# Kernel tuning notes

Hardware: AMD Instinct MI355X
Metric: run time of the kernel (lower is better)

Reference implementation:

```python
import jax, jax.numpy as jnp
import numpy as np

B, P, D, N = 16, 128, 256, 256  # batch, patches, channels (d), features (n); d <= n required


def setup_inputs() -> dict:
    key = jax.random.key(0)
    k1, k2, k3, k4 = jax.random.split(key, 4)
    x = jax.random.normal(k1, (B, P, D, N), dtype=jnp.float32)
    # Linear(n, 1) weights stacked over the d layers: W[i] is the i-th layer's weight row.
    bound = 1.0 / np.sqrt(N)
    W = jax.random.uniform(k2, (D, N), dtype=jnp.float32, minval=-bound, maxval=bound)
    bias = jax.random.uniform(k3, (D,), dtype=jnp.float32, minval=-bound, maxval=bound)
    # Each row of perm is an independent random permutation of [0, N) (matches torch.randperm per row).
    perm = jnp.argsort(jax.random.uniform(k4, (D, N)), axis=1).astype(jnp.int32)
    return {"x": x, "W": W, "bias": bias, "perm": perm}


def reference(x, W, bias, perm):
    # x: [b,p,d,n]; gather along last axis with a per-channel permutation: xp[b,p,i,k] = x[b,p,i,perm[i,k]]
    xp = jnp.take_along_axis(x, perm[None, None, :, :].astype(jnp.int32), axis=3)
    # Linear_i(n -> 1): y[b,p,i] = sum_k xp[b,p,i,k] * W[i,k] + bias[i]
    y = jnp.einsum('bpdn,dn->bpd', xp, W) + bias
    # The original inner j-loop writes the same scalar to every j: res[:,:,i,j] = y[:,:,i]
    return jnp.broadcast_to(y[..., None], x.shape)
```

## Files before the change

### kernel.cpp

```cpp
#include <hip/hip_runtime.h>

#define D_CH 256
#define N_F  256
#define ROWS_TOTAL 2048
#define CHUNKS 16
#define ROWS_PER_BLOCK (ROWS_TOTAL / CHUNKS)

typedef float f32x4 __attribute__((ext_vector_type(4)));

__global__ __launch_bounds__(256) void reuse_linear_kernel(
    const float* __restrict__ x,
    const float* __restrict__ W,
    const float* __restrict__ bias,
    const int*   __restrict__ perm,
    float*       __restrict__ out)
{
    __shared__ float wp[N_F];

    const int d     = blockIdx.x;
    const int chunk = blockIdx.y;
    const int tid   = threadIdx.x;

    wp[perm[d * N_F + tid]] = W[d * N_F + tid];
    __syncthreads();

    const int lane = tid & 63;
    const int wave = tid >> 6;

    const f32x4 w4 = *reinterpret_cast<const f32x4*>(&wp[lane * 4]);
    const float bv = bias[d];

    const int row0 = chunk * ROWS_PER_BLOCK + wave;
    const size_t row_stride4 = (size_t)4 * D_CH * N_F;

    #pragma unroll 2
    for (int i = 0; i < 32; i += 2) {
        const size_t b0 = ((size_t)(row0 + 4 * i) * D_CH + d) * N_F + lane * 4;
        const size_t b1 = b0 + row_stride4;

        const f32x4 a0 = __builtin_nontemporal_load(
            reinterpret_cast<const f32x4*>(x + b0));
        const f32x4 a1 = __builtin_nontemporal_load(
            reinterpret_cast<const f32x4*>(x + b1));

        float p0 = a0.x * w4.x + a0.y * w4.y + a0.z * w4.z + a0.w * w4.w;
        float p1 = a1.x * w4.x + a1.y * w4.y + a1.z * w4.z + a1.w * w4.w;

        #pragma unroll
        for (int m = 32; m >= 1; m >>= 1) {
            p0 += __shfl_xor(p0, m, 64);
            p1 += __shfl_xor(p1, m, 64);
        }

        const float y0 = p0 + bv;
        const float y1 = p1 + bv;
        f32x4 o0; o0.x = o0.y = o0.z = o0.w = y0;
        f32x4 o1; o1.x = o1.y = o1.z = o1.w = y1;
        __builtin_nontemporal_store(o0, reinterpret_cast<f32x4*>(out + b0));
        __builtin_nontemporal_store(o1, reinterpret_cast<f32x4*>(out + b1));
    }
}

extern "C" void kernel_launch(void* const* d_in, const int* in_sizes, int n_in,
                              void* d_out, int out_size, void* d_ws, size_t ws_size,
                              hipStream_t stream) {
    const float* x    = (const float*)d_in[0];
    const float* W    = (const float*)d_in[1];
    const float* bias = (const float*)d_in[2];
    const int*   perm = (const int*)d_in[3];
    float*       out  = (float*)d_out;

    dim3 grid(D_CH, CHUNKS);
    reuse_linear_kernel<<<grid, 256, 0, stream>>>(x, W, bias, perm, out);
}
```

Measured before the change: 825.8 us.

## Pre-permute W into workspace and stream contiguous rows per block

Adds a small kernel that scatters W through perm into a workspace buffer once. The main kernel then assigns one (b,p) row per block and walks channels in contiguous 1 KB segments, so each block reads and writes one contiguous 256 KB region instead of 1 KB pieces strided across rows. Nontemporal loads and stores are replaced by ordinary ones. The cost is an extra launch, and the permuted W is now reread from global memory or cache by every block. The old chunked kernel remains as a fallback when the workspace is too small.

```diff
diff --git a/kernel.cpp b/kernel.cpp
--- a/kernel.cpp
+++ b/kernel.cpp
@@ -3,12 +3,62 @@
 #define D_CH 256
 #define N_F  256
 #define ROWS_TOTAL 2048
-#define CHUNKS 16
-#define ROWS_PER_BLOCK (ROWS_TOTAL / CHUNKS)
 
 typedef float f32x4 __attribute__((ext_vector_type(4)));
 
-__global__ __launch_bounds__(256) void reuse_linear_kernel(
+__global__ __launch_bounds__(256) void permute_w_kernel(
+    const float* __restrict__ W,
+    const int*   __restrict__ perm,
+    float*       __restrict__ Wp)
+{
+    const int i = blockIdx.x * 256 + threadIdx.x;
+    const int d = i >> 8;
+    Wp[(d << 8) + perm[i]] = W[i];
+}
+
+__global__ __launch_bounds__(256) void reuse_linear_rows_kernel(
+    const float* __restrict__ x,
+    const float* __restrict__ Wp,
+    const float* __restrict__ bias,
+    float*       __restrict__ out)
+{
+    const int r    = blockIdx.x;
+    const int lane = threadIdx.x & 63;
+    const int wave = threadIdx.x >> 6;
+
+    const size_t rowbase = (size_t)r * D_CH * N_F;
+    const int    li4     = lane * 4;
+
+    for (int s0 = wave; s0 < D_CH; s0 += 8) {
+        const int s1 = s0 + 4;
+
+        const size_t xo0 = rowbase + (size_t)s0 * N_F + li4;
+        const size_t xo1 = rowbase + (size_t)s1 * N_F + li4;
+
+        const f32x4 a0 = *reinterpret_cast<const f32x4*>(x  + xo0);
+        const f32x4 a1 = *reinterpret_cast<const f32x4*>(x  + xo1);
+        const f32x4 w0 = *reinterpret_cast<const f32x4*>(Wp + (size_t)s0 * N_F + li4);
+        const f32x4 w1 = *reinterpret_cast<const f32x4*>(Wp + (size_t)s1 * N_F + li4);
+
+        float p0 = a0.x * w0.x + a0.y * w0.y + a0.z * w0.z + a0.w * w0.w;
+        float p1 = a1.x * w1.x + a1.y * w1.y + a1.z * w1.z + a1.w * w1.w;
+
+        #pragma unroll
+        for (int m = 32; m >= 1; m >>= 1) {
+            p0 += __shfl_xor(p0, m, 64);
+            p1 += __shfl_xor(p1, m, 64);
+        }
+
+        const float y0 = p0 + bias[s0];
+        const float y1 = p1 + bias[s1];
+        f32x4 o0; o0.x = o0.y = o0.z = o0.w = y0;
+        f32x4 o1; o1.x = o1.y = o1.z = o1.w = y1;
+        *reinterpret_cast<f32x4*>(out + xo0) = o0;
+        *reinterpret_cast<f32x4*>(out + xo1) = o1;
+    }
+}
+
+__global__ __launch_bounds__(256) void reuse_linear_chunk_kernel(
     const float* __restrict__ x,
     const float* __restrict__ W,
     const float* __restrict__ bias,
@@ -16,7 +66,6 @@
     float*       __restrict__ out)
 {
     __shared__ float wp[N_F];
-
     const int d     = blockIdx.x;
     const int chunk = blockIdx.y;
     const int tid   = threadIdx.x;
@@ -26,38 +75,19 @@
 
     const int lane = tid & 63;
     const int wave = tid >> 6;
-
     const f32x4 w4 = *reinterpret_cast<const f32x4*>(&wp[lane * 4]);
     const float bv = bias[d];
 
-    const int row0 = chunk * ROWS_PER_BLOCK + wave;
-    const size_t row_stride4 = (size_t)4 * D_CH * N_F;
-
-    #pragma unroll 2
-    for (int i = 0; i < 32; i += 2) {
-        const size_t b0 = ((size_t)(row0 + 4 * i) * D_CH + d) * N_F + lane * 4;
-        const size_t b1 = b0 + row_stride4;
-
-        const f32x4 a0 = __builtin_nontemporal_load(
-            reinterpret_cast<const f32x4*>(x + b0));
-        const f32x4 a1 = __builtin_nontemporal_load(
-            reinterpret_cast<const f32x4*>(x + b1));
-
-        float p0 = a0.x * w4.x + a0.y * w4.y + a0.z * w4.z + a0.w * w4.w;
-        float p1 = a1.x * w4.x + a1.y * w4.y + a1.z * w4.z + a1.w * w4.w;
-
+    const int row0 = chunk * (ROWS_TOTAL / 16) + wave;
+    for (int i = 0; i < 32; ++i) {
+        const size_t base = ((size_t)(row0 + 4 * i) * D_CH + d) * N_F + lane * 4;
+        const f32x4 x4 = *reinterpret_cast<const f32x4*>(x + base);
+        float p = x4.x * w4.x + x4.y * w4.y + x4.z * w4.z + x4.w * w4.w;
         #pragma unroll
-        for (int m = 32; m >= 1; m >>= 1) {
-            p0 += __shfl_xor(p0, m, 64);
-            p1 += __shfl_xor(p1, m, 64);
-        }
-
-        const float y0 = p0 + bv;
-        const float y1 = p1 + bv;
-        f32x4 o0; o0.x = o0.y = o0.z = o0.w = y0;
-        f32x4 o1; o1.x = o1.y = o1.z = o1.w = y1;
-        __builtin_nontemporal_store(o0, reinterpret_cast<f32x4*>(out + b0));
-        __builtin_nontemporal_store(o1, reinterpret_cast<f32x4*>(out + b1));
+        for (int m = 32; m >= 1; m >>= 1) p += __shfl_xor(p, m, 64);
+        const float y = p + bv;
+        f32x4 o; o.x = o.y = o.z = o.w = y;
+        *reinterpret_cast<f32x4*>(out + base) = o;
     }
 }
 
@@ -70,6 +100,13 @@
     const int*   perm = (const int*)d_in[3];
     float*       out  = (float*)d_out;
 
-    dim3 grid(D_CH, CHUNKS);
-    reuse_linear_kernel<<<grid, 256, 0, stream>>>(x, W, bias, perm, out);
+    const size_t wp_bytes = (size_t)D_CH * N_F * sizeof(float);
+    if (ws_size >= wp_bytes) {
+        float* Wp = (float*)d_ws;
+        permute_w_kernel<<<D_CH, 256, 0, stream>>>(W, perm, Wp);
+        reuse_linear_rows_kernel<<<ROWS_TOTAL, 256, 0, stream>>>(x, Wp, bias, out);
+    } else {
+        dim3 grid(D_CH, 16);
+        reuse_linear_chunk_kernel<<<grid, 256, 0, stream>>>(x, W, bias, perm, out);
+    }
 }
```

After: 861.2 us. 1.04x slower.
